# Performance work log

Hardware: AMD Instinct MI355X
Metric: run time of the kernel (lower is better)

The kernel has to match this reference:

```python
import jax, jax.numpy as jnp
import numpy as np

D = 768
H = 16
DH = D // H  # 48


def setup_inputs() -> dict:
    key = jax.random.key(0)
    ks = jax.random.split(key, 7)
    s = 0.02
    x = jax.random.normal(ks[0], (4, 2048, D), dtype=jnp.float32)
    # weights stored as (in, out); torch Linear is y = x @ W.T + b
    W_qkv = jax.random.normal(ks[1], (D, 3 * D), dtype=jnp.float32) * s
    b_qkv = jax.random.normal(ks[2], (3 * D,), dtype=jnp.float32) * s
    W_o = jax.random.normal(ks[3], (D, D), dtype=jnp.float32) * s
    b_o = jax.random.normal(ks[4], (D,), dtype=jnp.float32) * s
    W_p = jax.random.normal(ks[5], (D, D), dtype=jnp.float32) * s
    b_p = jax.random.normal(ks[6], (D,), dtype=jnp.float32) * s
    return {"x": x, "W_qkv": W_qkv, "b_qkv": b_qkv, "W_o": W_o, "b_o": b_o, "W_p": W_p, "b_p": b_p}


def reference(x, W_qkv, b_qkv, W_o, b_o, W_p, b_p):
    b, n, _ = x.shape
    qkv = x @ W_qkv + b_qkv                     # (b, n, 3*D)
    # reshape to (b, n, H, 3*DH) as in torch, then chunk last dim into q,k,v
    # -> per-head interleaved layout [q_h | k_h | v_h]
    qkv = qkv.reshape(b, n, H, 3, DH).transpose(0, 2, 1, 3, 4)  # (b, H, n, 3, DH)
    q, k, v = qkv[..., 0, :], qkv[..., 1, :], qkv[..., 2, :]    # (b, H, n, DH)
    alpha = jnp.einsum("bhqd,bhkd->bhqk", q, k) / jnp.sqrt(jnp.float32(DH))
    alpha = jax.nn.softmax(alpha, axis=-1)      # dropout: eval mode (identity)
    out = jnp.einsum("bhqk,bhkd->bhqd", alpha, v)
    out = out.transpose(0, 2, 1, 3).reshape(b, n, D)
    out = out @ W_o + b_o
    out = out @ W_p + b_p
    return out
```

## Files before the change

kernel.cpp:

```cpp
#include <hip/hip_runtime.h>

#define DEV __device__ __forceinline__

typedef __attribute__((ext_vector_type(4))) float f32x4;
typedef __attribute__((ext_vector_type(8))) short bf16x8;
typedef __attribute__((ext_vector_type(4))) short bf16x4;
typedef __attribute__((ext_vector_type(4))) unsigned int u32x4;

DEV short f2bf(float f) {
  union { float f; unsigned u; } c; c.f = f;
  unsigned r = c.u + 0x7FFFu + ((c.u >> 16) & 1u);
  return (short)(r >> 16);
}

DEV unsigned cvtpk(float lo, float hi) {
  unsigned r;
  asm("v_cvt_pk_bf16_f32 %0, %1, %2" : "=v"(r) : "v"(lo), "v"(hi));
  return r;
}

DEV float exp2r(float x) { return __builtin_amdgcn_exp2f(x); }

DEV void gl_lds16(short* lds, const short* g) {
  __builtin_amdgcn_global_load_lds(
      (__attribute__((address_space(1))) void*)(void*)g,
      (__attribute__((address_space(3))) void*)lds, 16, 0, 0);
}

DEV int xcd_swz(int orig, int nwg) {
  int q = nwg >> 3, r = nwg & 7;
  int xcd = orig & 7, idx = orig >> 3;
  return (xcd < r ? xcd * (q + 1) : r * (q + 1) + (xcd - r) * q) + idx;
}

__global__ __launch_bounds__(256) void k_cvt2(const float* __restrict__ in1, short* __restrict__ out1,
                                              int nb1, const float* __restrict__ in2, short* __restrict__ out2) {
  int b = blockIdx.x;
  const float* in = in1; short* out = out1;
  if (b >= nb1) { in = in2; out = out2; b -= nb1; }
  int i = b * 256 + threadIdx.x;
  float4 v = reinterpret_cast<const float4*>(in)[i];
  bf16x4 o;
  o[0] = f2bf(v.x); o[1] = f2bf(v.y); o[2] = f2bf(v.z); o[3] = f2bf(v.w);
  reinterpret_cast<bf16x4*>(out)[i] = o;
}

__global__ __launch_bounds__(256) void k_tcvt(const float* __restrict__ W, short* __restrict__ WT,
                                              int Kd, int Nd) {
  __shared__ float t[32][33];
  int nb = blockIdx.x * 32, kb = blockIdx.y * 32;
  int tx = threadIdx.x, ty = threadIdx.y;
#pragma unroll
  for (int i = ty; i < 32; i += 8) t[i][tx] = W[(long)(kb + i) * Nd + nb + tx];
  __syncthreads();
#pragma unroll
  for (int i = ty; i < 32; i += 8) WT[(long)(nb + i) * Kd + kb + tx] = f2bf(t[tx][i]);
}

__global__ __launch_bounds__(256) void k_bias(const float* __restrict__ bo, const float* __restrict__ bp,
                                              const float* __restrict__ Wp, float* __restrict__ bc) {
  int j = blockIdx.x * 256 + threadIdx.x;
  int k0 = blockIdx.y * 48;
  float s = 0.f;
#pragma unroll
  for (int k = 0; k < 48; ++k) s += bo[k0 + k] * Wp[(long)(k0 + k) * 768 + j];
  if (blockIdx.y == 0) s += bp[j];
  atomicAdd(&bc[j], s);
}

__global__ __launch_bounds__(512, 1) void k_gemm8(
    const short* __restrict__ A, const short* __restrict__ BT, const float* __restrict__ bias,
    short* __restrict__ Qp, short* __restrict__ Kp, short* __restrict__ VT, int K) {
  __shared__ short As[2][256 * 64];
  __shared__ short Bs[2][128 * 64];
  const int tid = threadIdx.x;
  const int w = tid >> 6, lane = tid & 63;
  const int lr = lane & 15, g = lane >> 4;
  const int r_l = lane >> 3, c_l = lane & 7;
  const int gsw = (c_l ^ r_l) * 8;

  const int nbx = gridDim.x;
  int lin = blockIdx.y * nbx + blockIdx.x;
  lin = xcd_swz(lin, nbx * gridDim.y);
  const int bx = lin % nbx, by = lin / nbx;
  const int m0 = by * 256, n0 = bx * 128;
  const int wm = (w >> 1) * 64, wn = (w & 1) * 64;

  f32x4 acc[4][4];
#pragma unroll
  for (int i = 0; i < 4; ++i)
#pragma unroll
    for (int j = 0; j < 4; ++j)
#pragma unroll
      for (int r = 0; r < 4; ++r) acc[i][j][r] = 0.f;

  const short* Ab = A + (long)m0 * K;
  const short* Bb = BT + (long)n0 * K;
  const int nk = K >> 6;

  auto STAGE_A = [&](int s, int kt, int j) {
    int rowb = j * 64 + w * 8;
    gl_lds16(&As[s][rowb * 64], Ab + (long)(rowb + r_l) * K + (kt << 6) + gsw);
  };
  auto STAGE_B = [&](int s, int kt, int j) {
    int rowb = j * 64 + w * 8;
    gl_lds16(&Bs[s][rowb * 64], Bb + (long)(rowb + r_l) * K + (kt << 6) + gsw);
  };

  STAGE_A(0, 0, 0); STAGE_A(0, 0, 1); STAGE_A(0, 0, 2); STAGE_A(0, 0, 3);
  STAGE_B(0, 0, 0); STAGE_B(0, 0, 1);

  for (int kt = 0; kt < nk; ++kt) {
    const int cur = kt & 1, ns = cur ^ 1;
    const bool pre = (kt + 1 < nk);
    asm volatile("s_waitcnt vmcnt(0)" ::: "memory");
    __builtin_amdgcn_s_barrier();

    const short* AsC = As[cur];
    const short* BsC = Bs[cur];

    bf16x8 bf[4][2];
    bf16x8 af[2];
#pragma unroll
    for (int p = 0; p < 4; ++p) {
      if (p == 0) {
#pragma unroll
        for (int nj = 0; nj < 4; ++nj) {
          int r = wn + nj * 16 + lr;
          const short* rb = BsC + r * 64;
          bf[nj][0] = *reinterpret_cast<const bf16x8*>(rb + ((0 + g) ^ (r & 7)) * 8);
          bf[nj][1] = *reinterpret_cast<const bf16x8*>(rb + ((4 + g) ^ (r & 7)) * 8);
        }
      }
      {
        int r = wm + p * 16 + lr;
        const short* ra = AsC + r * 64;
        af[0] = *reinterpret_cast<const bf16x8*>(ra + ((0 + g) ^ (r & 7)) * 8);
        af[1] = *reinterpret_cast<const bf16x8*>(ra + ((4 + g) ^ (r & 7)) * 8);
      }
      if (pre) {
        if (p == 0)      { STAGE_A(ns, kt + 1, 0); STAGE_A(ns, kt + 1, 1); }
        else if (p == 1) { STAGE_A(ns, kt + 1, 2); STAGE_A(ns, kt + 1, 3); }
        else if (p == 2) { STAGE_B(ns, kt + 1, 0); STAGE_B(ns, kt + 1, 1); }
      }
      __builtin_amdgcn_s_barrier();
      __builtin_amdgcn_s_setprio(1);
#pragma unroll
      for (int nj = 0; nj < 4; ++nj) {
        acc[p][nj] = __builtin_amdgcn_mfma_f32_16x16x32_bf16(af[0], bf[nj][0], acc[p][nj], 0, 0, 0);
        acc[p][nj] = __builtin_amdgcn_mfma_f32_16x16x32_bf16(af[1], bf[nj][1], acc[p][nj], 0, 0, 0);
      }
      __builtin_amdgcn_s_setprio(0);
      if (p < 3) __builtin_amdgcn_s_barrier();
    }
  }

#pragma unroll
  for (int nj = 0; nj < 4; ++nj) {
    int col = n0 + wn + nj * 16 + lr;
    float bv = bias[col];
    int h = col / 144;
    int rem = col - h * 144;
    int s = rem / 48;
    int d = rem - s * 48;
#pragma unroll
    for (int mi = 0; mi < 4; ++mi)
#pragma unroll
      for (int r = 0; r < 4; ++r) {
        int row = m0 + wm + mi * 16 + g * 4 + r;
        float val = acc[mi][nj][r] + bv;
        int b = row >> 11, n = row & 2047;
        int bh = (b << 4) + h;
        if (s == 0) {
          long o = ((long)(bh * 2048 + n)) * 64 + d;
          Qp[o] = f2bf(val * 0.20823051649867783f);
          if (d < 16) Qp[o + 48] = 0;
        } else if (s == 1) {
          long o = ((long)(bh * 2048 + n)) * 64 + d;
          Kp[o] = f2bf(val);
          if (d < 16) Kp[o + 48] = 0;
        } else {
          VT[((long)(bh * 48 + d)) * 2048 + n] = f2bf(val);
        }
      }
  }
}

template <int MODE>
__global__ __launch_bounds__(256) void k_gemm(
    const short* __restrict__ A, const short* __restrict__ BT, const float* __restrict__ bias,
    short* __restrict__ Cb, float* __restrict__ Cf, int M, int N, int K) {
  __shared__ short As[3][128 * 32];
  __shared__ short Bs[3][128 * 32];
  const int tid = threadIdx.x;
  const int w = tid >> 6, lane = tid & 63;
  const int lr = lane & 15, g = lane >> 4;

  const int nbx = gridDim.x;
  int lin = blockIdx.y * nbx + blockIdx.x;
  lin = xcd_swz(lin, nbx * gridDim.y);
  const int bx = lin % nbx, by = lin / nbx;
  const int m0 = by * 128, n0 = bx * 128;
  const int wm = (w >> 1) * 64, wn = (w & 1) * 64;

  f32x4 acc[4][4];
#pragma unroll
  for (int i = 0; i < 4; ++i)
#pragma unroll
    for (int j = 0; j < 4; ++j)
#pragma unroll
      for (int r = 0; r < 4; ++r) acc[i][j][r] = 0.f;

  const short* Ab = A + (long)m0 * K;
  const short* Bb = BT + (long)n0 * K;
  const int row_s = tid >> 2;
  const int c_s = tid & 3;
  const int nk = K >> 5;

  auto STAGE = [&](int b, int kt) {
    const int k0 = kt << 5;
#pragma unroll
    for (int i = 0; i < 2; ++i) {
      int row = row_s + i * 64;
      int cs = c_s ^ ((row >> 1) & 3);
      gl_lds16(&As[b][(i * 256 + w * 64) * 8], Ab + (long)row * K + k0 + cs * 8);
      gl_lds16(&Bs[b][(i * 256 + w * 64) * 8], Bb + (long)row * K + k0 + cs * 8);
    }
  };

  STAGE(0, 0);
  STAGE(1, 1);

  for (int kt = 0; kt < nk; ++kt) {
    if (kt < nk - 1) asm volatile("s_waitcnt vmcnt(4)" ::: "memory");
    else             asm volatile("s_waitcnt vmcnt(0)" ::: "memory");
    __builtin_amdgcn_s_barrier();

    if (kt + 2 < nk) STAGE((kt + 2) % 3, kt + 2);

    const short* AsC = As[kt % 3];
    const short* BsC = Bs[kt % 3];
    bf16x8 af[4], bf[4];
#pragma unroll
    for (int mi = 0; mi < 4; ++mi) {
      int r = wm + mi * 16 + lr;
      int c = g ^ ((r >> 1) & 3);
      af[mi] = *reinterpret_cast<const bf16x8*>(AsC + r * 32 + c * 8);
    }
#pragma unroll
    for (int nj = 0; nj < 4; ++nj) {
      int r = wn + nj * 16 + lr;
      int c = g ^ ((r >> 1) & 3);
      bf[nj] = *reinterpret_cast<const bf16x8*>(BsC + r * 32 + c * 8);
    }
    __builtin_amdgcn_s_setprio(1);
#pragma unroll
    for (int mi = 0; mi < 4; ++mi)
#pragma unroll
      for (int nj = 0; nj < 4; ++nj)
        acc[mi][nj] = __builtin_amdgcn_mfma_f32_16x16x32_bf16(af[mi], bf[nj], acc[mi][nj], 0, 0, 0);
    __builtin_amdgcn_s_setprio(0);
  }

#pragma unroll
  for (int nj = 0; nj < 4; ++nj) {
    int col = n0 + wn + nj * 16 + lr;
    float bv = (MODE == 3) ? 0.f : bias[col];
#pragma unroll
    for (int mi = 0; mi < 4; ++mi)
#pragma unroll
      for (int r = 0; r < 4; ++r) {
        int row = m0 + wm + mi * 16 + g * 4 + r;
        float val = acc[mi][nj][r] + bv;
        if (MODE == 2) Cf[(long)row * N + col] = val;
        else           Cb[(long)row * N + col] = f2bf(val);
      }
  }
}

__global__ __launch_bounds__(256, 4) void k_attn(const short* __restrict__ Q, const short* __restrict__ K,
                                                 const short* __restrict__ VT, short* __restrict__ AO) {
  const int tid = threadIdx.x, w = tid >> 6, lane = tid & 63;
  const int lr = lane & 15, g = lane >> 4;
  const int orig = blockIdx.x;
  const int logical = (orig & 7) * 128 + (orig >> 3);
  const int bh = logical >> 4;
  const int q0 = (logical & 15) * 128 + w * 32;

  const short* Qh = Q + (long)bh * 2048 * 64;
  const short* Kh = K + (long)bh * 2048 * 64;
  const short* VTh = VT + (long)bh * 48 * 2048;

  __shared__ short Ks[2][64 * 64];
  __shared__ short Vs[2][48 * 64];

  const int r_l = lane >> 3, c_l = lane & 7;
  const int gc8 = (c_l ^ r_l) * 8;

  bf16x8 bq0 = *reinterpret_cast<const bf16x8*>(Qh + (q0 + lr) * 64 + g * 8);
  bf16x8 bq1 = *reinterpret_cast<const bf16x8*>(Qh + (q0 + lr) * 64 + 32 + g * 8);
  bf16x8 bq2 = *reinterpret_cast<const bf16x8*>(Qh + (q0 + 16 + lr) * 64 + g * 8);
  bf16x8 bq3 = *reinterpret_cast<const bf16x8*>(Qh + (q0 + 16 + lr) * 64 + 32 + g * 8);

  bf16x8 vones;
#pragma unroll
  for (int i = 0; i < 8; ++i) vones[i] = (short)0x3F80;

  f32x4 accA[3], accB[3];
#pragma unroll
  for (int df = 0; df < 3; ++df)
#pragma unroll
    for (int r = 0; r < 4; ++r) { accA[df][r] = 0.f; accB[df][r] = 0.f; }
  f32x4 acclA = {0.f, 0.f, 0.f, 0.f}, acclB = {0.f, 0.f, 0.f, 0.f};

  const short* kg = Kh + (long)(w * 8 + r_l) * 64 + gc8;
  const short* vg = VTh + (long)(w * 8 + r_l) * 2048 + gc8;

  auto STAGE = [&](int b) {
    gl_lds16(&Ks[b][w * 512], kg);
    gl_lds16(&Ks[b][(w + 4) * 512], kg + 2048);
    gl_lds16(&Vs[b][w * 512], vg);
    if (w < 2) gl_lds16(&Vs[b][(w + 4) * 512], vg + 65536);
  };

  STAGE(0);
  kg += 4096; vg += 64;
  asm volatile("s_waitcnt vmcnt(0)" ::: "memory");
  __syncthreads();

  const int sw = lr & 7;
  const int goff = (g & 1) * 4;
  const int ghalf = g >> 1;

  for (int t = 0; t < 32; ++t) {
    const int cur = t & 1;
    if (t < 31) {
      STAGE(cur ^ 1);
      kg += 4096; vg += 64;
    }

    const short* KsC = Ks[cur];
    const short* VsC = Vs[cur];

    f32x4 stA[4], stB[4];
    __builtin_amdgcn_s_setprio(1);
#pragma unroll
    for (int kf = 0; kf < 4; ++kf) {
      const short* kr = KsC + (kf * 16 + lr) * 64;
      bf16x8 a0 = *reinterpret_cast<const bf16x8*>(kr + (g ^ sw) * 8);
      bf16x8 a1 = *reinterpret_cast<const bf16x8*>(kr + ((4 + g) ^ sw) * 8);
      f32x4 sA = {0.f, 0.f, 0.f, 0.f}, sB = {0.f, 0.f, 0.f, 0.f};
      sA = __builtin_amdgcn_mfma_f32_16x16x32_bf16(a0, bq0, sA, 0, 0, 0);
      sB = __builtin_amdgcn_mfma_f32_16x16x32_bf16(a0, bq2, sB, 0, 0, 0);
      sA = __builtin_amdgcn_mfma_f32_16x16x32_bf16(a1, bq1, sA, 0, 0, 0);
      sB = __builtin_amdgcn_mfma_f32_16x16x32_bf16(a1, bq3, sB, 0, 0, 0);
      stA[kf] = sA; stB[kf] = sB;
    }
    __builtin_amdgcn_s_setprio(0);

#pragma unroll
    for (int kf = 0; kf < 4; ++kf)
#pragma unroll
      for (int r = 0; r < 4; ++r) {
        stA[kf][r] = exp2r(stA[kf][r]);
        stB[kf][r] = exp2r(stB[kf][r]);
      }

    __builtin_amdgcn_s_setprio(1);
#pragma unroll
    for (int ks = 0; ks < 2; ++ks) {
      u32x4 bwA, bwB;
      bwA[0] = cvtpk(stA[2 * ks][0], stA[2 * ks][1]);
      bwA[1] = cvtpk(stA[2 * ks][2], stA[2 * ks][3]);
      bwA[2] = cvtpk(stA[2 * ks + 1][0], stA[2 * ks + 1][1]);
      bwA[3] = cvtpk(stA[2 * ks + 1][2], stA[2 * ks + 1][3]);
      bwB[0] = cvtpk(stB[2 * ks][0], stB[2 * ks][1]);
      bwB[1] = cvtpk(stB[2 * ks][2], stB[2 * ks][3]);
      bwB[2] = cvtpk(stB[2 * ks + 1][0], stB[2 * ks + 1][1]);
      bwB[3] = cvtpk(stB[2 * ks + 1][2], stB[2 * ks + 1][3]);
      bf16x8 bpA = __builtin_bit_cast(bf16x8, bwA);
      bf16x8 bpB = __builtin_bit_cast(bf16x8, bwB);
      const int off_lo = ((ks * 4 + ghalf) ^ sw) * 8 + goff;
      const int off_hi = ((ks * 4 + 2 + ghalf) ^ sw) * 8 + goff;
      acclA = __builtin_amdgcn_mfma_f32_16x16x32_bf16(vones, bpA, acclA, 0, 0, 0);
      acclB = __builtin_amdgcn_mfma_f32_16x16x32_bf16(vones, bpB, acclB, 0, 0, 0);
#pragma unroll
      for (int df = 0; df < 3; ++df) {
        const short* vbase = VsC + (df * 16 + lr) * 64;
        union { bf16x8 v; bf16x4 h[2]; } av;
        av.h[0] = *reinterpret_cast<const bf16x4*>(vbase + off_lo);
        av.h[1] = *reinterpret_cast<const bf16x4*>(vbase + off_hi);
        accA[df] = __builtin_amdgcn_mfma_f32_16x16x32_bf16(av.v, bpA, accA[df], 0, 0, 0);
        accB[df] = __builtin_amdgcn_mfma_f32_16x16x32_bf16(av.v, bpB, accB[df], 0, 0, 0);
      }
    }
    __builtin_amdgcn_s_setprio(0);

    asm volatile("s_waitcnt vmcnt(0)" ::: "memory");
    __syncthreads();
  }

  int b = bh >> 4, h = bh & 15;
  float invA = 1.f / acclA[0];
  float invB = 1.f / acclB[0];
  long rowA = ((long)((b << 11) + q0 + lr)) * 768 + h * 48;
  long rowB = ((long)((b << 11) + q0 + 16 + lr)) * 768 + h * 48;
#pragma unroll
  for (int df = 0; df < 3; ++df) {
    bf16x4 oA, oB;
#pragma unroll
    for (int r = 0; r < 4; ++r) { oA[r] = f2bf(accA[df][r] * invA); oB[r] = f2bf(accB[df][r] * invB); }
    *reinterpret_cast<bf16x4*>(AO + rowA + df * 16 + g * 4) = oA;
    *reinterpret_cast<bf16x4*>(AO + rowB + df * 16 + g * 4) = oB;
  }
}

extern "C" void kernel_launch(void* const* d_in, const int* in_sizes, int n_in,
                              void* d_out, int out_size, void* d_ws, size_t ws_size,
                              hipStream_t stream) {
  const float* x    = (const float*)d_in[0];
  const float* Wqkv = (const float*)d_in[1];
  const float* bqkv = (const float*)d_in[2];
  const float* Wo   = (const float*)d_in[3];
  const float* bo   = (const float*)d_in[4];
  const float* Wp   = (const float*)d_in[5];
  const float* bp   = (const float*)d_in[6];

  char* ws = (char*)d_ws;
  short* xb    = (short*)(ws + 0);
  short* WqkvT = (short*)(ws + 12582912);
  short* Wob   = (short*)(ws + 16121856);
  short* WpT   = (short*)(ws + 17301504);
  short* Qp    = (short*)(ws + 18481152);
  short* Kp    = (short*)(ws + 35258368);
  short* VT    = (short*)(ws + 52035584);
  short* AO    = (short*)(ws + 64618496);
  short* WoWpT = (short*)(ws + 2097152);
  float* bc    = (float*)(ws + 4194304);

  k_cvt2<<<6720, 256, 0, stream>>>(x, xb, 6144, Wo, Wob);
  k_tcvt<<<dim3(72, 24), dim3(32, 8), 0, stream>>>(Wqkv, WqkvT, 768, 2304);
  k_tcvt<<<dim3(24, 24), dim3(32, 8), 0, stream>>>(Wp, WpT, 768, 768);

  k_gemm8<<<dim3(18, 32), 512, 0, stream>>>(xb, WqkvT, bqkv, Qp, Kp, VT, 768);

  k_gemm<3><<<dim3(6, 6), 256, 0, stream>>>(WpT, Wob, nullptr, WoWpT, nullptr, 768, 768, 768);
  hipMemsetAsync(bc, 0, 768 * sizeof(float), stream);
  k_bias<<<dim3(3, 16), 256, 0, stream>>>(bo, bp, Wp, bc);

  k_attn<<<1024, 256, 0, stream>>>(Qp, Kp, VT, AO);
  k_gemm<2><<<dim3(6, 64), 256, 0, stream>>>(AO, WoWpT, bc, nullptr, (float*)d_out, 8192, 768, 768);
}
```

Before: 196.6 us.

## Use shared 256x256-tile GEMM kernel for QKV and output projections

Replaces the 256x128 QKV GEMM with a templated 256x256-tile kernel using K-step 32 and a simpler single-barrier double-buffered loop, and reuses it for the final output projection instead of the 128x128 kernel. Larger tiles raise data reuse per LDS load, and the single barrier per K step cuts synchronisation. The cost is fewer blocks (288 and 96), which may underfill the GPU's compute units, plus higher register pressure from the 4x8 accumulator.

```diff
diff --git a/kernel.cpp b/kernel.cpp
--- a/kernel.cpp
+++ b/kernel.cpp
@@ -68,121 +68,117 @@
   atomicAdd(&bc[j], s);
 }
 
-__global__ __launch_bounds__(512, 1) void k_gemm8(
+template <int MODE>
+__global__ __launch_bounds__(512, 2) void k_gemm256(
     const short* __restrict__ A, const short* __restrict__ BT, const float* __restrict__ bias,
-    short* __restrict__ Qp, short* __restrict__ Kp, short* __restrict__ VT, int K) {
-  __shared__ short As[2][256 * 64];
-  __shared__ short Bs[2][128 * 64];
+    float* __restrict__ Cf,
+    short* __restrict__ Qp, short* __restrict__ Kp, short* __restrict__ VT,
+    int N, int K) {
+  __shared__ short As[2][256 * 32];
+  __shared__ short Bs[2][256 * 32];
   const int tid = threadIdx.x;
   const int w = tid >> 6, lane = tid & 63;
   const int lr = lane & 15, g = lane >> 4;
-  const int r_l = lane >> 3, c_l = lane & 7;
-  const int gsw = (c_l ^ r_l) * 8;
+  const int row4 = lane >> 2;
+  const int cs8 = ((lane & 3) ^ ((lane >> 3) & 3)) * 8;
 
   const int nbx = gridDim.x;
   int lin = blockIdx.y * nbx + blockIdx.x;
   lin = xcd_swz(lin, nbx * gridDim.y);
   const int bx = lin % nbx, by = lin / nbx;
-  const int m0 = by * 256, n0 = bx * 128;
-  const int wm = (w >> 1) * 64, wn = (w & 1) * 64;
-
-  f32x4 acc[4][4];
+  const int m0 = by * 256, n0 = bx * 256;
+  const int wm = (w >> 1) * 64, wn = (w & 1) * 128;
+
+  f32x4 acc[4][8];
 #pragma unroll
   for (int i = 0; i < 4; ++i)
 #pragma unroll
-    for (int j = 0; j < 4; ++j)
+    for (int j = 0; j < 8; ++j)
 #pragma unroll
       for (int r = 0; r < 4; ++r) acc[i][j][r] = 0.f;
 
   const short* Ab = A + (long)m0 * K;
   const short* Bb = BT + (long)n0 * K;
-  const int nk = K >> 6;
-
-  auto STAGE_A = [&](int s, int kt, int j) {
-    int rowb = j * 64 + w * 8;
-    gl_lds16(&As[s][rowb * 64], Ab + (long)(rowb + r_l) * K + (kt << 6) + gsw);
+  const int nk = K >> 5;
+
+  auto STAGE = [&](int s, int kt) {
+    const int k0 = kt << 5;
+    int r0 = w * 16;
+    gl_lds16(&As[s][r0 * 32],         Ab + (long)(r0 + row4) * K + k0 + cs8);
+    gl_lds16(&As[s][(128 + r0) * 32], Ab + (long)(128 + r0 + row4) * K + k0 + cs8);
+    gl_lds16(&Bs[s][r0 * 32],         Bb + (long)(r0 + row4) * K + k0 + cs8);
+    gl_lds16(&Bs[s][(128 + r0) * 32], Bb + (long)(128 + r0 + row4) * K + k0 + cs8);
   };
-  auto STAGE_B = [&](int s, int kt, int j) {
-    int rowb = j * 64 + w * 8;
-    gl_lds16(&Bs[s][rowb * 64], Bb + (long)(rowb + r_l) * K + (kt << 6) + gsw);
-  };
-
-  STAGE_A(0, 0, 0); STAGE_A(0, 0, 1); STAGE_A(0, 0, 2); STAGE_A(0, 0, 3);
-  STAGE_B(0, 0, 0); STAGE_B(0, 0, 1);
+
+  STAGE(0, 0);
 
   for (int kt = 0; kt < nk; ++kt) {
-    const int cur = kt & 1, ns = cur ^ 1;
-    const bool pre = (kt + 1 < nk);
     asm volatile("s_waitcnt vmcnt(0)" ::: "memory");
     __builtin_amdgcn_s_barrier();
-
-    const short* AsC = As[cur];
-    const short* BsC = Bs[cur];
-
-    bf16x8 bf[4][2];
-    bf16x8 af[2];
-#pragma unroll
-    for (int p = 0; p < 4; ++p) {
-      if (p == 0) {
-#pragma unroll
-        for (int nj = 0; nj < 4; ++nj) {
-          int r = wn + nj * 16 + lr;
-          const short* rb = BsC + r * 64;
-          bf[nj][0] = *reinterpret_cast<const bf16x8*>(rb + ((0 + g) ^ (r & 7)) * 8);
-          bf[nj][1] = *reinterpret_cast<const bf16x8*>(rb + ((4 + g) ^ (r & 7)) * 8);
-        }
-      }
-      {
-        int r = wm + p * 16 + lr;
-        const short* ra = AsC + r * 64;
-        af[0] = *reinterpret_cast<const bf16x8*>(ra + ((0 + g) ^ (r & 7)) * 8);
-        af[1] = *reinterpret_cast<const bf16x8*>(ra + ((4 + g) ^ (r & 7)) * 8);
-      }
-      if (pre) {
-        if (p == 0)      { STAGE_A(ns, kt + 1, 0); STAGE_A(ns, kt + 1, 1); }
-        else if (p == 1) { STAGE_A(ns, kt + 1, 2); STAGE_A(ns, kt + 1, 3); }
-        else if (p == 2) { STAGE_B(ns, kt + 1, 0); STAGE_B(ns, kt + 1, 1); }
-      }
-      __builtin_amdgcn_s_barrier();
-      __builtin_amdgcn_s_setprio(1);
-#pragma unroll
-      for (int nj = 0; nj < 4; ++nj) {
-        acc[p][nj] = __builtin_amdgcn_mfma_f32_16x16x32_bf16(af[0], bf[nj][0], acc[p][nj], 0, 0, 0);
-        acc[p][nj] = __builtin_amdgcn_mfma_f32_16x16x32_bf16(af[1], bf[nj][1], acc[p][nj], 0, 0, 0);
-      }
-      __builtin_amdgcn_s_setprio(0);
-      if (p < 3) __builtin_amdgcn_s_barrier();
-    }
-  }
-
-#pragma unroll
-  for (int nj = 0; nj < 4; ++nj) {
+    if (kt + 1 < nk) STAGE((kt + 1) & 1, kt + 1);
+
+    const short* AsC = As[kt & 1];
+    const short* BsC = Bs[kt & 1];
+    bf16x8 af[4], bf[8];
+#pragma unroll
+    for (int mi = 0; mi < 4; ++mi) {
+      int r = wm + mi * 16 + lr;
+      int c = g ^ ((r >> 1) & 3);
+      af[mi] = *reinterpret_cast<const bf16x8*>(AsC + r * 32 + c * 8);
+    }
+#pragma unroll
+    for (int nj = 0; nj < 8; ++nj) {
+      int r = wn + nj * 16 + lr;
+      int c = g ^ ((r >> 1) & 3);
+      bf[nj] = *reinterpret_cast<const bf16x8*>(BsC + r * 32 + c * 8);
+    }
+    __builtin_amdgcn_s_setprio(1);
+#pragma unroll
+    for (int mi = 0; mi < 4; ++mi)
+#pragma unroll
+      for (int nj = 0; nj < 8; ++nj)
+        acc[mi][nj] = __builtin_amdgcn_mfma_f32_16x16x32_bf16(af[mi], bf[nj], acc[mi][nj], 0, 0, 0);
+    __builtin_amdgcn_s_setprio(0);
+  }
+
+#pragma unroll
+  for (int nj = 0; nj < 8; ++nj) {
     int col = n0 + wn + nj * 16 + lr;
     float bv = bias[col];
-    int h = col / 144;
-    int rem = col - h * 144;
-    int s = rem / 48;
-    int d = rem - s * 48;
-#pragma unroll
-    for (int mi = 0; mi < 4; ++mi)
-#pragma unroll
-      for (int r = 0; r < 4; ++r) {
-        int row = m0 + wm + mi * 16 + g * 4 + r;
-        float val = acc[mi][nj][r] + bv;
-        int b = row >> 11, n = row & 2047;
-        int bh = (b << 4) + h;
-        if (s == 0) {
-          long o = ((long)(bh * 2048 + n)) * 64 + d;
-          Qp[o] = f2bf(val * 0.20823051649867783f);
-          if (d < 16) Qp[o + 48] = 0;
-        } else if (s == 1) {
-          long o = ((long)(bh * 2048 + n)) * 64 + d;
-          Kp[o] = f2bf(val);
-          if (d < 16) Kp[o + 48] = 0;
-        } else {
-          VT[((long)(bh * 48 + d)) * 2048 + n] = f2bf(val);
+    if (MODE == 0) {
+      int h = col / 144;
+      int rem = col - h * 144;
+      int s = rem / 48;
+      int d = rem - s * 48;
+#pragma unroll
+      for (int mi = 0; mi < 4; ++mi)
+#pragma unroll
+        for (int r = 0; r < 4; ++r) {
+          int row = m0 + wm + mi * 16 + g * 4 + r;
+          float val = acc[mi][nj][r] + bv;
+          int b = row >> 11, n = row & 2047;
+          int bh = (b << 4) + h;
+          if (s == 0) {
+            long o = ((long)(bh * 2048 + n)) * 64 + d;
+            Qp[o] = f2bf(val * 0.20823051649867783f);
+            if (d < 16) Qp[o + 48] = 0;
+          } else if (s == 1) {
+            long o = ((long)(bh * 2048 + n)) * 64 + d;
+            Kp[o] = f2bf(val);
+            if (d < 16) Kp[o + 48] = 0;
+          } else {
+            VT[((long)(bh * 48 + d)) * 2048 + n] = f2bf(val);
+          }
         }
-      }
+    } else {
+#pragma unroll
+      for (int mi = 0; mi < 4; ++mi)
+#pragma unroll
+        for (int r = 0; r < 4; ++r) {
+          int row = m0 + wm + mi * 16 + g * 4 + r;
+          Cf[(long)row * N + col] = acc[mi][nj][r] + bv;
+        }
+    }
   }
 }
 
@@ -442,12 +438,13 @@
   k_tcvt<<<dim3(72, 24), dim3(32, 8), 0, stream>>>(Wqkv, WqkvT, 768, 2304);
   k_tcvt<<<dim3(24, 24), dim3(32, 8), 0, stream>>>(Wp, WpT, 768, 768);
 
-  k_gemm8<<<dim3(18, 32), 512, 0, stream>>>(xb, WqkvT, bqkv, Qp, Kp, VT, 768);
-
+  k_gemm256<0><<<dim3(9, 32), 512, 0, stream>>>(xb, WqkvT, bqkv, nullptr,
+                                                Qp, Kp, VT, 2304, 768);
   k_gemm<3><<<dim3(6, 6), 256, 0, stream>>>(WpT, Wob, nullptr, WoWpT, nullptr, 768, 768, 768);
   hipMemsetAsync(bc, 0, 768 * sizeof(float), stream);
   k_bias<<<dim3(3, 16), 256, 0, stream>>>(bo, bp, Wp, bc);
 
   k_attn<<<1024, 256, 0, stream>>>(Qp, Kp, VT, AO);
-  k_gemm<2><<<dim3(6, 64), 256, 0, stream>>>(AO, WoWpT, bc, nullptr, (float*)d_out, 8192, 768, 768);
-}
+  k_gemm256<2><<<dim3(3, 32), 512, 0, stream>>>(AO, WoWpT, bc, (float*)d_out,
+                                                nullptr, nullptr, nullptr, 768, 768);
+}
```

Measured after the change: 222.8 us. 13.3% more time.
